# Performance work log

Hardware: AMD Instinct MI355X
Metric: run time of the kernel (lower is better)

The kernel has to match this reference:

```python
import jax, jax.numpy as jnp
import numpy as np

LR, HR, H, D1 = 512, 2048, 4, 200
N = 2 * HR            # 4096 nodes (fully connected graph)
C1 = D1 // H          # 50  per-head dim, layer 1
C2 = HR // H          # 512 per-head dim, layer 2
EPS = 1e-5


def setup_inputs() -> dict:
    key = jax.random.key(0)
    ks = jax.random.split(key, 24)
    lin = lambda k, fi, fo: jax.random.normal(k, (fi, fo), jnp.float32) * 0.02
    vec = lambda k, d: jax.random.normal(k, (d,), jnp.float32) * 0.02
    inp = {"lr_x": jax.random.normal(ks[0], (LR, N), jnp.float32)}
    # TransformerConv 1: lr -> 200 (query/key/value/skip linears, each with bias)
    inp["Wq1"], inp["bq1"] = lin(ks[1], LR, D1), vec(ks[2], D1)
    inp["Wk1"], inp["bk1"] = lin(ks[3], LR, D1), vec(ks[4], D1)
    inp["Wv1"], inp["bv1"] = lin(ks[5], LR, D1), vec(ks[6], D1)
    inp["Ws1"], inp["bs1"] = lin(ks[7], LR, D1), vec(ks[8], D1)
    # GraphNorm 1
    inp["gn1_w"] = 1.0 + 0.1 * jax.random.normal(ks[9], (D1,), jnp.float32)
    inp["gn1_b"] = vec(ks[10], D1)
    inp["gn1_ms"] = 1.0 + 0.1 * jax.random.normal(ks[11], (D1,), jnp.float32)
    # TransformerConv 2: 200 -> 2048
    inp["Wq2"], inp["bq2"] = lin(ks[12], D1, HR), vec(ks[13], HR)
    inp["Wk2"], inp["bk2"] = lin(ks[14], D1, HR), vec(ks[15], HR)
    inp["Wv2"], inp["bv2"] = lin(ks[16], D1, HR), vec(ks[17], HR)
    inp["Ws2"], inp["bs2"] = lin(ks[18], D1, HR), vec(ks[19], HR)
    # GraphNorm 2
    inp["gn2_w"] = 1.0 + 0.1 * jax.random.normal(ks[20], (HR,), jnp.float32)
    inp["gn2_b"] = vec(ks[21], HR)
    inp["gn2_ms"] = 1.0 + 0.1 * jax.random.normal(ks[22], (HR,), jnp.float32)
    return inp


def _transformer_conv(x, Wq, bq, Wk, bk, Wv, bv, Ws, bs, heads, ch):
    # PyG TransformerConv on a fully-connected edge_index == dense multi-head attention
    n = x.shape[0]
    q = (x @ Wq + bq).reshape(n, heads, ch)
    k = (x @ Wk + bk).reshape(n, heads, ch)
    v = (x @ Wv + bv).reshape(n, heads, ch)
    scores = jnp.einsum('ihc,jhc->hij', q, k) / (ch ** 0.5)  # [H, N, N]
    attn = jax.nn.softmax(scores, axis=-1)                   # softmax over source nodes j
    out = jnp.einsum('hij,jhc->ihc', attn, v).reshape(n, heads * ch)
    return out + x @ Ws + bs                                 # root/skip connection


def _graph_norm(x, w, b, ms):
    # PyG GraphNorm: y = w * (x - ms*mean) / sqrt(E[(x - ms*mean)^2] + eps) + b
    mean = jnp.mean(x, axis=0, keepdims=True)
    out = x - mean * ms
    var = jnp.mean(out * out, axis=0, keepdims=True)
    return out * jax.lax.rsqrt(var + EPS) * w + b


def reference(lr_x, Wq1, bq1, Wk1, bk1, Wv1, bv1, Ws1, bs1, gn1_w, gn1_b, gn1_ms,
              Wq2, bq2, Wk2, bk2, Wv2, bv2, Ws2, bs2, gn2_w, gn2_b, gn2_ms):
    h = _transformer_conv(lr_x.T, Wq1, bq1, Wk1, bk1, Wv1, bv1, Ws1, bs1, H, C1)  # [N, 200]
    h = _graph_norm(h, gn1_w, gn1_b, gn1_ms)
    h2 = _transformer_conv(h, Wq2, bq2, Wk2, bk2, Wv2, bv2, Ws2, bs2, H, C2)      # [N, HR]
    h2 = _graph_norm(h2, gn2_w, gn2_b, gn2_ms).T                                  # [HR, N]
    h2 = h2 / jnp.linalg.norm(h2, axis=1, keepdims=True)
    return jax.nn.relu(h2 @ h2.T)                                                 # [HR, HR]
```

## Files before the change

### kernel.cpp

```cpp
#include <hip/hip_runtime.h>
#include <math.h>

typedef unsigned int u32;
typedef unsigned short ushort_t;
typedef __attribute__((ext_vector_type(8))) short short8;
typedef __attribute__((ext_vector_type(4))) float f32x4;

#define PRIO(x) __builtin_amdgcn_s_setprio(x)

__device__ __forceinline__ ushort_t f2bf(float x) {
  u32 u = __float_as_uint(x);
  u32 r = (u + 0x7fffu + ((u >> 16) & 1u)) >> 16;
  return (ushort_t)r;
}
__device__ __forceinline__ float bf2f(u32 s) {
  return __uint_as_float(s << 16);
}
__device__ __forceinline__ void ld4bf(const ushort_t* p, float* o) {
  uint2 u = *(const uint2*)p;
  o[0] = bf2f(u.x & 0xffffu); o[1] = bf2f(u.x >> 16);
  o[2] = bf2f(u.y & 0xffffu); o[3] = bf2f(u.y >> 16);
}

__device__ __forceinline__ float block_sum256(float v, float* red) {
  #pragma unroll
  for (int o = 32; o > 0; o >>= 1) v += __shfl_down(v, o, 64);
  __syncthreads();
  if ((threadIdx.x & 63) == 0) red[threadIdx.x >> 6] = v;
  __syncthreads();
  return red[0] + red[1] + red[2] + red[3];
}

__global__ __launch_bounds__(256) void fused_attn1(
    const ushort_t* __restrict__ qk, const ushort_t* __restrict__ v,
    float* __restrict__ oP, float* __restrict__ r1p, float scale)
{
  __shared__ ushort_t Kl[2][4096];
  __shared__ ushort_t Vl[2][4096];
  __shared__ ushort_t Pl[128][80];
  const int t = threadIdx.x;
  const int lane = t & 63;
  const int wv = t >> 6;
  const int h = blockIdx.y;
  const int m0 = blockIdx.x * 128;
  const int z = blockIdx.z;
  const int lr = lane & 15;
  const int hk = lane >> 4;

  short8 aq[2][2];
  #pragma unroll
  for (int qb = 0; qb < 2; ++qb) {
    const ushort_t* qrow = qk + (size_t)(m0 + wv * 32 + qb * 16 + lr) * 512 + h * 64;
    aq[qb][0] = *(const short8*)(qrow + hk * 8);
    aq[qb][1] = *(const short8*)(qrow + 32 + hk * 8);
  }

  f32x4 oAcc[4][2];
  #pragma unroll
  for (int i = 0; i < 4; ++i) {
    oAcc[i][0] = (f32x4){0.f, 0.f, 0.f, 0.f};
    oAcc[i][1] = (f32x4){0.f, 0.f, 0.f, 0.f};
  }
  float racc[2][4] = {{0.f,0.f,0.f,0.f},{0.f,0.f,0.f,0.f}};

  const size_t kbase = (size_t)256 + h * 64;

  auto stage = [&](int buf, int n0) {
    #pragma unroll
    for (int i = 0; i < 2; ++i) {
      const int st = t + i * 256;
      const int row = st >> 3, cS = st & 7;
      const int lc = cS ^ (row & 7);
      __builtin_amdgcn_global_load_lds(
          (const __attribute__((address_space(1))) u32*)(qk + (size_t)(n0 + row) * 512 + kbase + lc * 8),
          (__attribute__((address_space(3))) u32*)(&Kl[buf][st * 8]), 16, 0, 0);
      __builtin_amdgcn_global_load_lds(
          (const __attribute__((address_space(1))) u32*)(v + (size_t)(h * 128 + row) * 4096 + n0 + lc * 8),
          (__attribute__((address_space(3))) u32*)(&Vl[buf][st * 8]), 16, 0, 0);
    }
  };

  stage(0, z * 1024);
  __syncthreads();

  int cur = 0;
  for (int it = 0; it < 16; ++it) {
    if (it + 1 < 16) stage(cur ^ 1, z * 1024 + (it + 1) * 64);
    #pragma unroll
    for (int nf = 0; nf < 4; ++nf) {
      const int rl = nf * 16 + lr;
      const char* kb = (const char*)&Kl[cur][0] + rl * 128;
      short8 b0 = *(const short8*)(kb + ((hk ^ (rl & 7)) * 16));
      short8 b1 = *(const short8*)(kb + (((4 + hk) ^ (rl & 7)) * 16));
      #pragma unroll
      for (int qb = 0; qb < 2; ++qb) {
        f32x4 sa = (f32x4){0.f, 0.f, 0.f, 0.f};
        PRIO(1);
        sa = __builtin_amdgcn_mfma_f32_16x16x32_bf16(aq[qb][0], b0, sa, 0, 0, 0);
        sa = __builtin_amdgcn_mfma_f32_16x16x32_bf16(aq[qb][1], b1, sa, 0, 0, 0);
        PRIO(0);
        #pragma unroll
        for (int r = 0; r < 4; ++r) {
          float e = exp2f(sa[r] * scale);
          racc[qb][r] += e;
          Pl[wv * 32 + qb * 16 + hk * 4 + r][nf * 16 + lr] = f2bf(e);
        }
      }
    }
    short8 ap[2][2];
    #pragma unroll
    for (int qb = 0; qb < 2; ++qb) {
      ap[qb][0] = *(const short8*)&Pl[wv * 32 + qb * 16 + lr][hk * 8];
      ap[qb][1] = *(const short8*)&Pl[wv * 32 + qb * 16 + lr][32 + hk * 8];
    }
    #pragma unroll
    for (int ff = 0; ff < 4; ++ff) {
      const int rl = ff * 16 + lr;
      const char* vb = (const char*)&Vl[cur][0] + rl * 128;
      short8 b0 = *(const short8*)(vb + ((hk ^ (rl & 7)) * 16));
      short8 b1 = *(const short8*)(vb + (((4 + hk) ^ (rl & 7)) * 16));
      PRIO(1);
      #pragma unroll
      for (int qb = 0; qb < 2; ++qb) {
        oAcc[ff][qb] = __builtin_amdgcn_mfma_f32_16x16x32_bf16(ap[qb][0], b0, oAcc[ff][qb], 0, 0, 0);
        oAcc[ff][qb] = __builtin_amdgcn_mfma_f32_16x16x32_bf16(ap[qb][1], b1, oAcc[ff][qb], 0, 0, 0);
      }
      PRIO(0);
    }
    __syncthreads();
    cur ^= 1;
  }

  #pragma unroll
  for (int qb = 0; qb < 2; ++qb) {
    #pragma unroll
    for (int r = 0; r < 4; ++r) {
      racc[qb][r] += __shfl_xor(racc[qb][r], 1);
      racc[qb][r] += __shfl_xor(racc[qb][r], 2);
      racc[qb][r] += __shfl_xor(racc[qb][r], 4);
      racc[qb][r] += __shfl_xor(racc[qb][r], 8);
    }
  }
  if (lr == 0) {
    float* rp = r1p + ((size_t)z * 4 + h) * 4096;
    #pragma unroll
    for (int qb = 0; qb < 2; ++qb)
      #pragma unroll
      for (int r = 0; r < 4; ++r)
        rp[m0 + wv * 32 + qb * 16 + hk * 4 + r] = racc[qb][r];
  }
  float* ob = oP + (size_t)z * 512 * 4096;
  #pragma unroll
  for (int ff = 0; ff < 4; ++ff) {
    const size_t fbase = (size_t)(h * 128 + ff * 16 + lr) * 4096;
    #pragma unroll
    for (int qb = 0; qb < 2; ++qb)
      #pragma unroll
      for (int r = 0; r < 4; ++r)
        ob[fbase + m0 + wv * 32 + qb * 16 + hk * 4 + r] = oAcc[ff][qb][r];
  }
}

__global__ __launch_bounds__(512, 2) void fused_attn2(
    const ushort_t* __restrict__ Tm, const ushort_t* __restrict__ X,
    const ushort_t* __restrict__ Xt, ushort_t* __restrict__ Up, float scale)
{
  __shared__ ushort_t Xl[16384];
  __shared__ ushort_t Xtl[2][16384];
  __shared__ ushort_t Pl[256][72];
  const int t = threadIdx.x;
  const int lane = t & 63;
  const int wv = t >> 6;
  const int h = blockIdx.y;
  const int m0 = blockIdx.x * 256;
  const int z = blockIdx.z;
  const int lr = lane & 15;
  const int hk = lane >> 4;

  short8 tq[2][7];
  #pragma unroll
  for (int qb = 0; qb < 2; ++qb) {
    const ushort_t* trow = Tm + ((size_t)h * 4096 + m0 + wv * 32 + qb * 16 + lr) * 256;
    #pragma unroll
    for (int s = 0; s < 7; ++s) tq[qb][s] = *(const short8*)(trow + s * 32 + hk * 8);
  }

  f32x4 uAcc[14][2];
  #pragma unroll
  for (int i = 0; i < 14; ++i) {
    uAcc[i][0] = (f32x4){0.f, 0.f, 0.f, 0.f};
    uAcc[i][1] = (f32x4){0.f, 0.f, 0.f, 0.f};
  }

  auto stageX = [&](int n0) {
    #pragma unroll
    for (int i = 0; i < 4; ++i) {
      const int st = t + i * 512;
      const int row = st >> 5, ph = st & 31;
      const int lc = (ph & 24) | ((ph & 7) ^ (row & 7));
      __builtin_amdgcn_global_load_lds(
          (const __attribute__((address_space(1))) u32*)(X + (size_t)(n0 + row) * 256 + lc * 8),
          (__attribute__((address_space(3))) u32*)(&Xl[st * 8]), 16, 0, 0);
    }
  };
  auto stageXt = [&](int buf, int n0) {
    #pragma unroll
    for (int i = 0; i < 4; ++i) {
      const int st = t + i * 512;
      const int row = st >> 3, ph = st & 7;
      const int lc = ph ^ (row & 7);
      __builtin_amdgcn_global_load_lds(
          (const __attribute__((address_space(1))) u32*)(Xt + (size_t)row * 4096 + n0 + lc * 8),
          (__attribute__((address_space(3))) u32*)(&Xtl[buf][st * 8]), 16, 0, 0);
    }
  };

  const int base = z * 16;
  stageX(base * 64);
  stageXt(0, base * 64);
  __syncthreads();

  int cur = 0;
  for (int it = 0; it < 16; ++it) {
    if (it + 1 < 16) stageXt(cur ^ 1, (base + it + 1) * 64);
    const char* xb = (const char*)&Xl[0];
    #pragma unroll
    for (int nf = 0; nf < 4; ++nf) {
      const int row = nf * 16 + lr;
      const char* rb = xb + row * 512;
      f32x4 sa0 = (f32x4){0.f, 0.f, 0.f, 0.f};
      f32x4 sa1 = (f32x4){0.f, 0.f, 0.f, 0.f};
      PRIO(1);
      #pragma unroll
      for (int s = 0; s < 7; ++s) {
        const int c = s * 4 + hk;
        const int ph = (c & 24) | ((c & 7) ^ (row & 7));
        short8 xf = *(const short8*)(rb + ph * 16);
        sa0 = __builtin_amdgcn_mfma_f32_16x16x32_bf16(xf, tq[0][s], sa0, 0, 0, 0);
        sa1 = __builtin_amdgcn_mfma_f32_16x16x32_bf16(xf, tq[1][s], sa1, 0, 0, 0);
      }
      PRIO(0);
      uint2 w0, w1;
      w0.x = (u32)f2bf(exp2f(sa0[0] * scale)) | ((u32)f2bf(exp2f(sa0[1] * scale)) << 16);
      w0.y = (u32)f2bf(exp2f(sa0[2] * scale)) | ((u32)f2bf(exp2f(sa0[3] * scale)) << 16);
      w1.x = (u32)f2bf(exp2f(sa1[0] * scale)) | ((u32)f2bf(exp2f(sa1[1] * scale)) << 16);
      w1.y = (u32)f2bf(exp2f(sa1[2] * scale)) | ((u32)f2bf(exp2f(sa1[3] * scale)) << 16);
      *(uint2*)((char*)&Pl[wv * 32 + lr][0] + nf * 32 + hk * 8) = w0;
      *(uint2*)((char*)&Pl[wv * 32 + 16 + lr][0] + nf * 32 + hk * 8) = w1;
    }
    __syncthreads();
    if (it + 1 < 16) stageX((base + it + 1) * 64);
    short8 p00 = *(const short8*)((const char*)&Pl[wv * 32 + lr][0] + hk * 16);
    short8 p01 = *(const short8*)((const char*)&Pl[wv * 32 + lr][0] + (4 + hk) * 16);
    short8 p10 = *(const short8*)((const char*)&Pl[wv * 32 + 16 + lr][0] + hk * 16);
    short8 p11 = *(const short8*)((const char*)&Pl[wv * 32 + 16 + lr][0] + (4 + hk) * 16);
    const char* xtb = (const char*)&Xtl[cur][0];
    #pragma unroll
    for (int ff = 0; ff < 14; ++ff) {
      const int row = ff * 16 + lr;
      const char* rb2 = xtb + row * 128;
      short8 x0 = *(const short8*)(rb2 + ((hk ^ (row & 7)) * 16));
      short8 x1 = *(const short8*)(rb2 + (((4 + hk) ^ (row & 7)) * 16));
      PRIO(1);
      uAcc[ff][0] = __builtin_amdgcn_mfma_f32_16x16x32_bf16(x0, p00, uAcc[ff][0], 0, 0, 0);
      uAcc[ff][0] = __builtin_amdgcn_mfma_f32_16x16x32_bf16(x1, p01, uAcc[ff][0], 0, 0, 0);
      uAcc[ff][1] = __builtin_amdgcn_mfma_f32_16x16x32_bf16(x0, p10, uAcc[ff][1], 0, 0, 0);
      uAcc[ff][1] = __builtin_amdgcn_mfma_f32_16x16x32_bf16(x1, p11, uAcc[ff][1], 0, 0, 0);
      PRIO(0);
    }
    __syncthreads();
    cur ^= 1;
  }

  ushort_t* ub = Up + (size_t)(z * 4 + h) * 256 * 4096;
  #pragma unroll
  for (int ff = 0; ff < 14; ++ff) {
    #pragma unroll
    for (int qb = 0; qb < 2; ++qb) {
      #pragma unroll
      for (int r = 0; r < 4; ++r) {
        const int a = ff * 16 + hk * 4 + r;
        ub[(size_t)a * 4096 + m0 + wv * 32 + qb * 16 + lr] = f2bf(uAcc[ff][qb][r]);
      }
    }
  }
}

__global__ __launch_bounds__(256) void combine_u(
    const ushort_t* __restrict__ Up, ushort_t* __restrict__ Usum,
    float* __restrict__ r2)
{
  __shared__ float tl[64][65];
  const int t = threadIdx.x;
  const int qt = blockIdx.x;
  const int at = blockIdx.y;
  const int h  = blockIdx.z;
  const int c = t & 63;
  const int rb = t >> 6;
  const size_t PLN = (size_t)4 * 256 * 4096;
  #pragma unroll
  for (int i = 0; i < 16; ++i) {
    const int r = rb + i * 4;
    const int a = at * 64 + r;
    const int q = qt * 64 + c;
    const size_t i0 = ((size_t)h * 256 + a) * 4096 + q;
    float val = bf2f(Up[i0]) + bf2f(Up[PLN + i0])
              + bf2f(Up[2 * PLN + i0]) + bf2f(Up[3 * PLN + i0]);
    tl[r][c] = val;
    if (a == 200) r2[(size_t)h * 4096 + q] = val;
  }
  __syncthreads();
  #pragma unroll
  for (int i = 0; i < 16; ++i) {
    const int r = rb + i * 4;
    const int q = qt * 64 + r;
    const int a = at * 64 + c;
    Usum[((size_t)h * 4096 + q) * 256 + a] = f2bf(tl[c][r]);
  }
}

#define RD_A(bb, mm, cc) (*(const short8*)(lsAc + (bb)*32768 + arow + (mm)*2048 + (cc)))
#define RD_B(bb, nn, cc) (*(const short8*)(lsBc + (bb)*32768 + brow + (nn)*2048 + (cc)))

#define MM8(nn, bv) { \
  acc[0][nn] = __builtin_amdgcn_mfma_f32_16x16x32_bf16(a0, bv, acc[0][nn], 0,0,0); \
  acc[1][nn] = __builtin_amdgcn_mfma_f32_16x16x32_bf16(a1, bv, acc[1][nn], 0,0,0); \
  acc[2][nn] = __builtin_amdgcn_mfma_f32_16x16x32_bf16(a2, bv, acc[2][nn], 0,0,0); \
  acc[3][nn] = __builtin_amdgcn_mfma_f32_16x16x32_bf16(a3, bv, acc[3][nn], 0,0,0); \
  acc[4][nn] = __builtin_amdgcn_mfma_f32_16x16x32_bf16(a4, bv, acc[4][nn], 0,0,0); \
  acc[5][nn] = __builtin_amdgcn_mfma_f32_16x16x32_bf16(a5, bv, acc[5][nn], 0,0,0); \
  acc[6][nn] = __builtin_amdgcn_mfma_f32_16x16x32_bf16(a6, bv, acc[6][nn], 0,0,0); \
  acc[7][nn] = __builtin_amdgcn_mfma_f32_16x16x32_bf16(a7, bv, acc[7][nn], 0,0,0); }

#define STG(BASE, LD, LS, bb, hf, tt) { \
  _Pragma("unroll") \
  for (int ii = 0; ii < 2; ++ii) { \
    const int s_ = t + ii * 512; \
    const int r_ = s_ >> 3; \
    const int lc_ = (s_ & 7) ^ (r_ & 7); \
    __builtin_amdgcn_global_load_lds( \
      (const __attribute__((address_space(1))) u32*)((BASE) + (size_t)((hf) * 128 + r_) * (LD) + (size_t)(tt) * 64 + lc_ * 8), \
      (__attribute__((address_space(3))) u32*)(&(LS)[bb][(hf) * 8192 + s_ * 8]), 16, 0, 0); \
  } }

#define BAR() __builtin_amdgcn_s_barrier()

#define GRP(bf, tS1, tS2) { \
  a0=RD_A(bf,0,c0); a1=RD_A(bf,1,c0); a2=RD_A(bf,2,c0); a3=RD_A(bf,3,c0); \
  a4=RD_A(bf,4,c0); a5=RD_A(bf,5,c0); a6=RD_A(bf,6,c0); a7=RD_A(bf,7,c0); \
  b0=RD_B(bf,0,c0); b1=RD_B(bf,1,c0); \
  STG(Ab, lda, lsA, 1-(bf), 1, tS1); STG(Bb, ldb, lsB, 1-(bf), 0, tS1); \
  BAR(); PRIO(1); MM8(0, b0); MM8(1, b1); PRIO(0); BAR(); \
  b2=RD_B(bf,2,c0); b3=RD_B(bf,3,c0); \
  STG(Bb, ldb, lsB, 1-(bf), 1, tS1); \
  BAR(); PRIO(1); MM8(2, b2); MM8(3, b3); PRIO(0); BAR(); \
  a0=RD_A(bf,0,c1); a1=RD_A(bf,1,c1); a2=RD_A(bf,2,c1); a3=RD_A(bf,3,c1); \
  a4=RD_A(bf,4,c1); a5=RD_A(bf,5,c1); a6=RD_A(bf,6,c1); a7=RD_A(bf,7,c1); \
  b0=RD_B(bf,0,c1); b1=RD_B(bf,1,c1); \
  BAR(); PRIO(1); MM8(0, b0); MM8(1, b1); PRIO(0); BAR(); \
  b2=RD_B(bf,2,c1); b3=RD_B(bf,3,c1); \
  STG(Ab, lda, lsA, (bf), 0, tS2); \
  BAR(); PRIO(1); MM8(2, b2); MM8(3, b3); PRIO(0); \
  asm volatile("s_waitcnt vmcnt(2)" ::: "memory"); \
  BAR(); }

template<int CMODE, bool RELU>
__global__ __launch_bounds__(512, 2) void mfma256_8ph(
    const ushort_t* __restrict__ A, const ushort_t* __restrict__ B,
    void* __restrict__ Cv, int lda, int ldb, int ldc,
    int K, int zsplit, size_t zA, size_t zB, size_t zC,
    int bShift, size_t bHead, int Mvalid, float scale)
{
  __shared__ ushort_t lsA[2][16384];
  __shared__ ushort_t lsB[2][16384];
  const int t = threadIdx.x;
  const int gx = gridDim.x;
  const int nwg = gx * gridDim.y;
  const int bid = blockIdx.y * gx + blockIdx.x;
  const int qq = nwg >> 3, rr_ = nwg & 7;
  const int xcd = bid & 7, idx = bid >> 3;
  const int swz = (xcd < rr_ ? xcd * (qq + 1) : rr_ * (qq + 1) + (xcd - rr_) * qq) + idx;
  const int m0 = (swz / gx) * 256;
  const int n0 = (swz % gx) * 256;
  const int z = blockIdx.z;
  int Kc = K, kOff = 0;
  size_t aZ = 0, bZ = 0, cZ = 0;
  if (zsplit > 1) { Kc = K / zsplit; kOff = z * Kc; cZ = (size_t)z * zC; }
  else { aZ = (size_t)z * zA; bZ = (size_t)z * zB; cZ = (size_t)z * zC; }
  const ushort_t* Ab = A + aZ + (size_t)m0 * lda + kOff;
  const ushort_t* Bb = B + bZ + (size_t)n0 * ldb + kOff
                     + (bShift >= 0 ? (size_t)(m0 >> bShift) * bHead : 0);
  const int NT = Kc / 64;

  f32x4 acc[8][4];
  #pragma unroll
  for (int i = 0; i < 8; ++i)
    #pragma unroll
    for (int j = 0; j < 4; ++j) acc[i][j] = (f32x4){0.f, 0.f, 0.f, 0.f};

  const int lane = t & 63;
  const int wv = t >> 6;
  const int wr = (wv >> 2) * 128;
  const int wc = (wv & 3) * 64;
  const int lr = lane & 15;
  const int kc = lane >> 4;
  const int sw = lane & 7;
  const int c0 = (kc ^ sw) * 16;
  const int c1 = c0 ^ 64;
  const int arow = (wr + lr) * 128;
  const int brow = (wc + lr) * 128;
  const char* lsAc = (const char*)lsA;
  const char* lsBc = (const char*)lsB;

  short8 a0, a1, a2, a3, a4, a5, a6, a7, b0, b1, b2, b3;

  STG(Ab, lda, lsA, 0, 0, 0); STG(Ab, lda, lsA, 0, 1, 0);
  STG(Bb, ldb, lsB, 0, 0, 0); STG(Bb, ldb, lsB, 0, 1, 0);
  STG(Ab, lda, lsA, 1, 0, 1);
  asm volatile("s_waitcnt vmcnt(2)" ::: "memory");
  BAR();

  const int NITER = NT >> 1;
  for (int it = 0; it < NITER; ++it) {
    const int tb = 2 * it;
    const int s1 = tb + 1;
    const int s2 = (tb + 2 < NT) ? tb + 2 : 0;
    const int s3 = (tb + 3 < NT) ? tb + 3 : 0;
    GRP(0, s1, s2)
    GRP(1, s2, s3)
  }

  const int row4 = (lane >> 4) * 4;
  const int coln = lane & 15;
  float* Cf = (float*)Cv + cZ;
  ushort_t* Ch = (ushort_t*)Cv + cZ;
  #pragma unroll
  for (int m = 0; m < 8; ++m) {
    #pragma unroll
    for (int r = 0; r < 4; ++r) {
      const int gm = m0 + wr + m * 16 + row4 + r;
      const bool ok = gm < Mvalid;
      #pragma unroll
      for (int n = 0; n < 4; ++n) {
        const int gn = n0 + wc + n * 16 + coln;
        float v = acc[m][n][r] * scale;
        if (RELU) v = fmaxf(v, 0.f);
        if (ok) {
          if (CMODE == 0)      Cf[(size_t)gm * ldc + gn] = v;
          else if (CMODE == 1) Ch[(size_t)gm * ldc + gn] = f2bf(v);
          else                 atomicAdd(&Cf[(size_t)gm * ldc + gn], v);
        }
      }
    }
  }
}

#undef GRP
#undef STG
#undef MM8
#undef RD_A
#undef RD_B

template<int CMODE, bool RELU>
__global__ __launch_bounds__(256) void mfma_bt(
    const ushort_t* __restrict__ A, const ushort_t* __restrict__ B,
    void* __restrict__ Cv, int lda, int ldb, int ldc,
    int K, int Ksplit, size_t zA, size_t zB, size_t zC,
    int bShift, size_t bHead, int mMask, int Mvalid, float scale)
{
  __shared__ ushort_t lsA[2][128 * 32];
  __shared__ ushort_t lsB[2][128 * 32];
  const int t  = threadIdx.x;
  const int m0 = blockIdx.y * 128;
  const int n0 = blockIdx.x * 128;
  const int z = blockIdx.z;
  int Kc = K, kOff = 0;
  size_t aZ = 0, bZ = 0, cZ = 0;
  if (Ksplit > 1) { Kc = K / Ksplit; kOff = z * Kc; cZ = (size_t)z * zC; }
  else { aZ = (size_t)z * zA; bZ = (size_t)z * zB; cZ = (size_t)z * zC; }
  const int NT = (Kc + 31) / 32;
  const ushort_t* Ab = A + aZ + (size_t)m0 * lda + kOff;
  const ushort_t* Bb = B + bZ + (size_t)n0 * ldb + kOff
                     + (bShift >= 0 ? (size_t)(m0 >> bShift) * bHead : 0);
  const int cs = t & 3;

  f32x4 acc[4][4];
  #pragma unroll
  for (int i = 0; i < 4; ++i)
    #pragma unroll
    for (int j = 0; j < 4; ++j) acc[i][j] = (f32x4){0.f, 0.f, 0.f, 0.f};

  const int lane = t & 63;
  const int wv = t >> 6;
  const int wr = (wv >> 1) * 64;
  const int wc = (wv & 1) * 64;
  const int lr = lane & 15;
  const int kc = lane >> 4;

  int roffA[4], roffB[4];
  #pragma unroll
  for (int m = 0; m < 4; ++m) {
    int ra = wr + m * 16 + lr;
    roffA[m] = ra * 64 + ((kc ^ (ra & 3)) * 16);
    int rb = wc + m * 16 + lr;
    roffB[m] = rb * 64 + ((kc ^ (rb & 3)) * 16);
  }

  auto stage = [&](int buf, int kt) {
    const ushort_t* As = Ab + kt * 32;
    const ushort_t* Bs = Bb + kt * 32;
    #pragma unroll
    for (int i = 0; i < 2; ++i) {
      int s = t + i * 256;
      int r = s >> 2;
      int c = cs ^ (r & 3);
      __builtin_amdgcn_global_load_lds(
          (const __attribute__((address_space(1))) u32*)(As + (size_t)r * lda + c * 8),
          (__attribute__((address_space(3))) u32*)(&lsA[buf][s * 8]), 16, 0, 0);
    }
    #pragma unroll
    for (int i = 0; i < 2; ++i) {
      int s = t + i * 256;
      int r = s >> 2;
      int c = cs ^ (r & 3);
      __builtin_amdgcn_global_load_lds(
          (const __attribute__((address_space(1))) u32*)(Bs + (size_t)r * ldb + c * 8),
          (__attribute__((address_space(3))) u32*)(&lsB[buf][s * 8]), 16, 0, 0);
    }
  };

  stage(0, 0);
  __syncthreads();
  int cur = 0;
  for (int kt = 0; kt < NT; ++kt) {
    if (kt + 1 < NT) stage(cur ^ 1, kt + 1);
    short8 af[4], bfr[4];
    const char* baseA = (const char*)&lsA[cur][0];
    const char* baseB = (const char*)&lsB[cur][0];
    #pragma unroll
    for (int m = 0; m < 4; ++m) af[m]  = *(const short8*)(baseA + roffA[m]);
    #pragma unroll
    for (int n = 0; n < 4; ++n) bfr[n] = *(const short8*)(baseB + roffB[n]);
    PRIO(1);
    #pragma unroll
    for (int m = 0; m < 4; ++m)
      #pragma unroll
      for (int n = 0; n < 4; ++n)
        acc[m][n] = __builtin_amdgcn_mfma_f32_16x16x32_bf16(af[m], bfr[n], acc[m][n], 0, 0, 0);
    PRIO(0);
    __syncthreads();
    cur ^= 1;
  }

  const int row4 = (lane >> 4) * 4;
  const int coln = lane & 15;
  float* Cf = (float*)Cv + cZ;
  ushort_t* Ch = (ushort_t*)Cv + cZ;
  #pragma unroll
  for (int m = 0; m < 4; ++m) {
    #pragma unroll
    for (int r = 0; r < 4; ++r) {
      const int gm = m0 + wr + m * 16 + row4 + r;
      const bool ok = (mMask >= 0) ? ((gm & mMask) < Mvalid) : (gm < Mvalid);
      #pragma unroll
      for (int n = 0; n < 4; ++n) {
        const int gn = n0 + wc + n * 16 + coln;
        float v = acc[m][n][r] * scale;
        if (RELU) v = fmaxf(v, 0.f);
        if (ok) {
          if (CMODE == 0)      Cf[(size_t)gm * ldc + gn] = v;
          else if (CMODE == 1) Ch[(size_t)gm * ldc + gn] = f2bf(v);
          else                 atomicAdd(&Cf[(size_t)gm * ldc + gn], v);
        }
      }
    }
  }
}

__global__ __launch_bounds__(256) void wt_conv(
    const float* __restrict__ W, const float* __restrict__ bias,
    ushort_t* __restrict__ dst, int Mtot, int ldw, int Kv, int Kp,
    int PADH, int VALH)
{
  const int m = blockIdx.x;
  const int h = m / PADH, c0 = m % PADH;
  const int fout = h * VALH + c0;
  const bool valid = (c0 < VALH) && (fout < Mtot);
  for (int k = threadIdx.x; k < Kp; k += blockDim.x) {
    float v = 0.f;
    if (valid) {
      if (k < Kv) v = W[(size_t)k * ldw + fout];
      else if (k == Kv) v = bias[fout];
    }
    dst[(size_t)m * Kp + k] = f2bf(v);
  }
}

__global__ __launch_bounds__(256) void wt_trans(
    const float* __restrict__ W, const float* __restrict__ bias,
    ushort_t* __restrict__ dst)
{
  const int rid = blockIdx.x;
  const int h = rid >> 8, a = rid & 255;
  for (int f = threadIdx.x; f < 512; f += 256) {
    float v = 0.f;
    if (a < 200)       v = W[(size_t)a * 2048 + h * 512 + f];
    else if (a == 200) v = bias[h * 512 + f];
    dst[(size_t)rid * 512 + f] = f2bf(v);
  }
}

__global__ __launch_bounds__(256) void xt_conv(
    const float* __restrict__ h1nT, ushort_t* __restrict__ Xt)
{
  const int a = blockIdx.x;
  for (int q = threadIdx.x; q < 4096; q += 256) {
    float v = (a < 200) ? h1nT[(size_t)a * 4096 + q] : ((a == 200) ? 1.f : 0.f);
    Xt[(size_t)a * 4096 + q] = f2bf(v);
  }
}

__global__ __launch_bounds__(256) void trans_pad(
    const float* __restrict__ src, ushort_t* __restrict__ dst, int Kv, int Kp)
{
  __shared__ float tl[64][65];
  const int t = threadIdx.x;
  const int f0 = blockIdx.x * 64;
  const int i0 = blockIdx.y * 64;
  const int c = t & 63, rbase = t >> 6;
  #pragma unroll
  for (int it = 0; it < 16; ++it) {
    int r = rbase + it * 4;
    int f = f0 + r;
    tl[r][c] = (f < Kv) ? src[(size_t)f * 4096 + i0 + c] : 0.f;
  }
  __syncthreads();
  #pragma unroll
  for (int it = 0; it < 16; ++it) {
    int r = rbase + it * 4;
    int f = f0 + c;
    if (f < Kp) {
      float v = (f < Kv) ? tl[c][r] : ((f == Kv) ? 1.f : 0.f);
      dst[(size_t)(i0 + r) * Kp + f] = f2bf(v);
    }
  }
}

__global__ __launch_bounds__(256) void graph_norm_attn1(
    const ushort_t* __restrict__ skip, const float* __restrict__ oP,
    const float* __restrict__ r1p, float* __restrict__ out,
    const float* __restrict__ w, const float* __restrict__ b,
    const float* __restrict__ ms)
{
  __shared__ float red[4];
  const int t = threadIdx.x;
  const int row = blockIdx.x;
  const int h = row / 50;
  const int pr = h * 128 + row % 50;
  const ushort_t* sk = skip + (size_t)pr * 4096;
  const size_t OSTR = (size_t)512 * 4096;
  float v[16];
  float s = 0.f;
  #pragma unroll
  for (int e = 0; e < 4; ++e) {
    const int idx = t * 4 + 1024 * e;
    float a[4];
    ld4bf(&sk[idx], a);
    float4 o0 = *(const float4*)&oP[(size_t)pr * 4096 + idx];
    float4 o1 = *(const float4*)&oP[OSTR + (size_t)pr * 4096 + idx];
    float4 o2 = *(const float4*)&oP[2 * OSTR + (size_t)pr * 4096 + idx];
    float4 o3 = *(const float4*)&oP[3 * OSTR + (size_t)pr * 4096 + idx];
    float4 r0 = *(const float4*)&r1p[(size_t)h * 4096 + idx];
    float4 r1 = *(const float4*)&r1p[(size_t)(4 + h) * 4096 + idx];
    float4 r2 = *(const float4*)&r1p[(size_t)(8 + h) * 4096 + idx];
    float4 r3 = *(const float4*)&r1p[(size_t)(12 + h) * 4096 + idx];
    v[e*4+0] = a[0] + (o0.x + o1.x + o2.x + o3.x) / (r0.x + r1.x + r2.x + r3.x);
    v[e*4+1] = a[1] + (o0.y + o1.y + o2.y + o3.y) / (r0.y + r1.y + r2.y + r3.y);
    v[e*4+2] = a[2] + (o0.z + o1.z + o2.z + o3.z) / (r0.z + r1.z + r2.z + r3.z);
    v[e*4+3] = a[3] + (o0.w + o1.w + o2.w + o3.w) / (r0.w + r1.w + r2.w + r3.w);
    s += v[e*4+0] + v[e*4+1] + v[e*4+2] + v[e*4+3];
  }
  const float mean = block_sum256(s, red) * (1.f / 4096.f);
  const float sub = mean * ms[row];
  float s2 = 0.f;
  #pragma unroll
  for (int e = 0; e < 16; ++e) { v[e] -= sub; s2 += v[e] * v[e]; }
  const float var = block_sum256(s2, red) * (1.f / 4096.f);
  const float scl = rsqrtf(var + 1e-5f) * w[row];
  const float bb = b[row];
  float* y = out + (size_t)row * 4096;
  #pragma unroll
  for (int e = 0; e < 4; ++e) {
    float o0[4];
    #pragma unroll
    for (int q = 0; q < 4; ++q) o0[q] = v[e * 4 + q] * scl + bb;
    *(float4*)&y[t * 4 + 1024 * e] = *(float4*)&o0[0];
  }
}

__global__ __launch_bounds__(256) void graph_norm_attn2(
    const ushort_t* __restrict__ skip, const ushort_t* __restrict__ O,
    const float* __restrict__ r2, ushort_t* __restrict__ out,
    const float* __restrict__ w, const float* __restrict__ b,
    const float* __restrict__ ms)
{
  __shared__ float red[4];
  const int t = threadIdx.x;
  const int row = blockIdx.x;
  const ushort_t* sk = skip + (size_t)row * 4096;
  const ushort_t* pa = O + (size_t)row * 4096;
  const float* rr = r2 + (size_t)(row >> 9) * 4096;
  float v[16];
  float s = 0.f;
  #pragma unroll
  for (int e = 0; e < 4; ++e) {
    const int idx = t * 4 + 1024 * e;
    float a[4], oa[4];
    ld4bf(&sk[idx], a); ld4bf(&pa[idx], oa);
    float4 rv = *(const float4*)&rr[idx];
    v[e*4+0] = a[0] + oa[0] / rv.x;
    v[e*4+1] = a[1] + oa[1] / rv.y;
    v[e*4+2] = a[2] + oa[2] / rv.z;
    v[e*4+3] = a[3] + oa[3] / rv.w;
    s += v[e*4+0] + v[e*4+1] + v[e*4+2] + v[e*4+3];
  }
  const float mean = block_sum256(s, red) * (1.f / 4096.f);
  const float sub = mean * ms[row];
  float s2 = 0.f;
  #pragma unroll
  for (int e = 0; e < 16; ++e) { v[e] -= sub; s2 += v[e] * v[e]; }
  const float var = block_sum256(s2, red) * (1.f / 4096.f);
  const float scl = rsqrtf(var + 1e-5f) * w[row];
  const float bb = b[row];
  #pragma unroll
  for (int e = 0; e < 16; ++e) v[e] = v[e] * scl + bb;
  float s3 = 0.f;
  #pragma unroll
  for (int e = 0; e < 16; ++e) s3 += v[e] * v[e];
  const float osc = rsqrtf(block_sum256(s3, red));
  ushort_t* y = out + (size_t)row * 4096;
  #pragma unroll
  for (int e = 0; e < 4; ++e) {
    ushort_t o0[4];
    #pragma unroll
    for (int q = 0; q < 4; ++q) o0[q] = f2bf(v[e * 4 + q] * osc);
    *(ushort2*)&y[t * 4 + 1024 * e] = *(ushort2*)&o0[0];
    *(ushort2*)&y[t * 4 + 1024 * e + 2] = *(ushort2*)&o0[2];
  }
}

__global__ __launch_bounds__(256) void add4_relu_bf16(
    const ushort_t* __restrict__ g, float* __restrict__ out)
{
  const size_t i = (size_t)blockIdx.x * 256 + threadIdx.x;
  const size_t ss = (size_t)2048 * 2048;
  float a[4], b[4], c[4], d[4];
  ld4bf(&g[i * 4], a);
  ld4bf(&g[ss + i * 4], b);
  ld4bf(&g[2 * ss + i * 4], c);
  ld4bf(&g[3 * ss + i * 4], d);
  float4 o;
  o.x = fmaxf(a[0] + b[0] + c[0] + d[0], 0.f);
  o.y = fmaxf(a[1] + b[1] + c[1] + d[1], 0.f);
  o.z = fmaxf(a[2] + b[2] + c[2] + d[2], 0.f);
  o.w = fmaxf(a[3] + b[3] + c[3] + d[3], 0.f);
  ((float4*)out)[i] = o;
}

extern "C" void kernel_launch(void* const* d_in, const int* in_sizes, int n_in,
                              void* d_out, int out_size, void* d_ws, size_t ws_size,
                              hipStream_t stream)
{
  (void)in_sizes; (void)n_in; (void)out_size; (void)ws_size;
  const float* lr_x = (const float*)d_in[0];
  const float* Wq1 = (const float*)d_in[1];  const float* bq1 = (const float*)d_in[2];
  const float* Wk1 = (const float*)d_in[3];  const float* bk1 = (const float*)d_in[4];
  const float* Wv1 = (const float*)d_in[5];  const float* bv1 = (const float*)d_in[6];
  const float* Ws1 = (const float*)d_in[7];  const float* bs1 = (const float*)d_in[8];
  const float* gn1w = (const float*)d_in[9]; const float* gn1b = (const float*)d_in[10];
  const float* gn1ms = (const float*)d_in[11];
  const float* Wq2 = (const float*)d_in[12]; const float* bq2 = (const float*)d_in[13];
  const float* Wk2 = (const float*)d_in[14]; const float* bk2 = (const float*)d_in[15];
  const float* Wv2 = (const float*)d_in[16]; const float* bv2 = (const float*)d_in[17];
  const float* Ws2 = (const float*)d_in[18]; const float* bs2 = (const float*)d_in[19];
  const float* gn2w = (const float*)d_in[20]; const float* gn2b = (const float*)d_in[21];
  const float* gn2ms = (const float*)d_in[22];

  char* p = (char*)d_ws;
  auto alloc = [&](size_t bytes) { char* r = p; p += (bytes + 255) & ~(size_t)255; return r; };
  char*     scrA = alloc((size_t)32 * 1024 * 1024);
  ushort_t* xb   = (ushort_t*)alloc((size_t)4096 * 544 * 2);
  ushort_t* qk1b = (ushort_t*)alloc((size_t)4096 * 512 * 2);
  ushort_t* v1s  = (ushort_t*)alloc((size_t)1024 * 4096 * 2);
  char*     u0   = alloc((size_t)16 * 1024 * 1024);
  float*    h1nT = (float*)   alloc((size_t)200 * 4096 * 4);
  ushort_t* h1nb = (ushort_t*)alloc((size_t)4096 * 256 * 2);
  ushort_t* Wqk1 = (ushort_t*)alloc((size_t)512 * 544 * 2);
  ushort_t* Wvs1 = (ushort_t*)alloc((size_t)1024 * 544 * 2);
  ushort_t* Wcat = (ushort_t*)alloc((size_t)4096 * 256 * 2);
  ushort_t* Qt   = (ushort_t*)alloc((size_t)4 * 256 * 512 * 2);
  ushort_t* Kt   = (ushort_t*)alloc((size_t)4 * 256 * 512 * 2);
  ushort_t* Mtall= (ushort_t*)alloc((size_t)4 * 256 * 256 * 2);
  ushort_t* Tall = (ushort_t*)alloc((size_t)4 * 4096 * 256 * 2);
  ushort_t* Xtb  = (ushort_t*)alloc((size_t)256 * 4096 * 2);
  ushort_t* vs2b = (ushort_t*)alloc((size_t)4096 * 4096 * 2);
  ushort_t* Usum = (ushort_t*)alloc((size_t)4 * 4096 * 256 * 2);
  ushort_t* Opl  = (ushort_t*)alloc((size_t)2048 * 4096 * 2);
  float*    r1p  = (float*)   alloc((size_t)16 * 4096 * 4);
  float*    r2   = (float*)   alloc((size_t)4 * 4096 * 4);
  float*    oP   = (float*)scrA;
  ushort_t* UpH  = (ushort_t*)scrA;
  ushort_t* g4   = (ushort_t*)scrA;
  ushort_t* h2b  = (ushort_t*)u0;

  const dim3 b256(256, 1, 1);
  const dim3 b512(512, 1, 1);
  const float LOG2E = 1.4426950408889634f;
  const float sc1e = 0.14142135623730951f * LOG2E;
  const float sc2e = 0.04419417382415922f * LOG2E;

  wt_conv<<<dim3(256),  b256, 0, stream>>>(Wq1, bq1, Wqk1,             200, 200, 512, 544, 64, 50);
  wt_conv<<<dim3(256),  b256, 0, stream>>>(Wk1, bk1, Wqk1 + 256 * 544, 200, 200, 512, 544, 64, 50);
  wt_conv<<<dim3(512),  b256, 0, stream>>>(Wv1, bv1, Wvs1,             200, 200, 512, 544, 128, 50);
  wt_conv<<<dim3(512),  b256, 0, stream>>>(Ws1, bs1, Wvs1 + 512 * 544, 200, 200, 512, 544, 128, 50);
  wt_conv<<<dim3(2048), b256, 0, stream>>>(Wv2, bv2, Wcat,              2048, 2048, 200, 256, 2048, 2048);
  wt_conv<<<dim3(2048), b256, 0, stream>>>(Ws2, bs2, Wcat + 2048 * 256, 2048, 2048, 200, 256, 2048, 2048);
  wt_trans<<<dim3(1024), b256, 0, stream>>>(Wq2, bq2, Qt);
  wt_trans<<<dim3(1024), b256, 0, stream>>>(Wk2, bk2, Kt);
  trans_pad<<<dim3(9, 64), b256, 0, stream>>>(lr_x, xb, 512, 544);

  mfma_bt<1, false><<<dim3(4, 32), b256, 0, stream>>>(
      xb, Wqk1, qk1b, 544, 544, 512, 544, 1, 0, 0, 0, -1, 0, -1, 4096, 1.f);
  mfma_bt<1, false><<<dim3(32, 8), b256, 0, stream>>>(
      Wvs1, xb, v1s, 544, 544, 4096, 544, 1, 0, 0, 0, -1, 0, -1, 1024, 1.f);

  fused_attn1<<<dim3(32, 4, 4), b256, 0, stream>>>(qk1b, v1s, oP, r1p, sc1e);
  graph_norm_attn1<<<dim3(200), b256, 0, stream>>>(
      v1s + (size_t)512 * 4096, oP, r1p, h1nT, gn1w, gn1b, gn1ms);
  trans_pad<<<dim3(4, 64), b256, 0, stream>>>(h1nT, h1nb, 200, 256);
  xt_conv<<<dim3(256), b256, 0, stream>>>(h1nT, Xtb);

  mfma_bt<1, false><<<dim3(32, 32), b256, 0, stream>>>(
      Wcat, h1nb, vs2b, 256, 256, 4096, 224, 1, 0, 0, 0, -1, 0, -1, 4096, 1.f);

  mfma_bt<1, false><<<dim3(2, 2, 4), b256, 0, stream>>>(
      Kt, Qt, Mtall, 512, 512, 256, 512, 1,
      (size_t)256 * 512, (size_t)256 * 512, (size_t)256 * 256, -1, 0, -1, 256, 1.f);
  mfma_bt<1, false><<<dim3(2, 32, 4), b256, 0, stream>>>(
      h1nb, Mtall, Tall, 256, 256, 256, 224, 1,
      0, (size_t)256 * 256, (size_t)4096 * 256, -1, 0, -1, 4096, 1.f);
  fused_attn2<<<dim3(16, 4, 4), b512, 0, stream>>>(Tall, h1nb, Xtb, UpH, sc2e);
  combine_u<<<dim3(64, 4, 4), b256, 0, stream>>>(UpH, Usum, r2);
  mfma_bt<1, false><<<dim3(32, 16), b256, 0, stream>>>(
      Wcat, Usum, Opl, 256, 256, 4096, 224, 1,
      0, 0, 0, 9, (size_t)4096 * 256, -1, 2048, 1.f);
  graph_norm_attn2<<<dim3(2048), b256, 0, stream>>>(
      vs2b + (size_t)2048 * 4096, Opl, r2, h2b, gn2w, gn2b, gn2ms);

  mfma256_8ph<1, false><<<dim3(8, 8, 4), b512, 0, stream>>>(
      h2b, h2b, g4, 4096, 4096, 2048, 4096, 4,
      0, 0, (size_t)2048 * 2048, -1, 0, 2048, 1.f);
  add4_relu_bf16<<<dim3(4096), b256, 0, stream>>>(g4, (float*)d_out);
}
```

Measured before the change: 325.4 us.

## Store attention partials in bf16, merge weight conversion launches, fuse Xt padding into norm

```diff
diff --git a/kernel.cpp b/kernel.cpp
--- a/kernel.cpp
+++ b/kernel.cpp
@@ -33,7 +33,7 @@
 
 __global__ __launch_bounds__(256) void fused_attn1(
     const ushort_t* __restrict__ qk, const ushort_t* __restrict__ v,
-    float* __restrict__ oP, float* __restrict__ r1p, float scale)
+    ushort_t* __restrict__ oP, float* __restrict__ r1p, float scale)
 {
   __shared__ ushort_t Kl[2][4096];
   __shared__ ushort_t Vl[2][4096];
@@ -149,15 +149,18 @@
       for (int r = 0; r < 4; ++r)
         rp[m0 + wv * 32 + qb * 16 + hk * 4 + r] = racc[qb][r];
   }
-  float* ob = oP + (size_t)z * 512 * 4096;
+  ushort_t* ob = oP + (size_t)z * 512 * 4096;
   #pragma unroll
   for (int ff = 0; ff < 4; ++ff) {
     const size_t fbase = (size_t)(h * 128 + ff * 16 + lr) * 4096;
     #pragma unroll
-    for (int qb = 0; qb < 2; ++qb)
-      #pragma unroll
-      for (int r = 0; r < 4; ++r)
-        ob[fbase + m0 + wv * 32 + qb * 16 + hk * 4 + r] = oAcc[ff][qb][r];
+    for (int qb = 0; qb < 2; ++qb) {
+      const int q0 = m0 + wv * 32 + qb * 16 + hk * 4;
+      uint2 w;
+      w.x = (u32)f2bf(oAcc[ff][qb][0]) | ((u32)f2bf(oAcc[ff][qb][1]) << 16);
+      w.y = (u32)f2bf(oAcc[ff][qb][2]) | ((u32)f2bf(oAcc[ff][qb][3]) << 16);
+      *(uint2*)&ob[fbase + q0] = w;
+    }
   }
 }
 
@@ -577,11 +580,14 @@
   }
 }
 
-__global__ __launch_bounds__(256) void wt_conv(
-    const float* __restrict__ W, const float* __restrict__ bias,
-    ushort_t* __restrict__ dst, int Mtot, int ldw, int Kv, int Kp,
-    int PADH, int VALH)
-{
+__global__ __launch_bounds__(256) void wt_conv2(
+    const float* __restrict__ W0, const float* __restrict__ b0v, ushort_t* __restrict__ d0,
+    const float* __restrict__ W1, const float* __restrict__ b1v, ushort_t* __restrict__ d1,
+    int Mtot, int ldw, int Kv, int Kp, int PADH, int VALH)
+{
+  const float* W = blockIdx.y ? W1 : W0;
+  const float* bias = blockIdx.y ? b1v : b0v;
+  ushort_t* dst = blockIdx.y ? d1 : d0;
   const int m = blockIdx.x;
   const int h = m / PADH, c0 = m % PADH;
   const int fout = h * VALH + c0;
@@ -596,10 +602,13 @@
   }
 }
 
-__global__ __launch_bounds__(256) void wt_trans(
-    const float* __restrict__ W, const float* __restrict__ bias,
-    ushort_t* __restrict__ dst)
-{
+__global__ __launch_bounds__(256) void wt_trans2(
+    const float* __restrict__ W0, const float* __restrict__ b0v, ushort_t* __restrict__ d0,
+    const float* __restrict__ W1, const float* __restrict__ b1v, ushort_t* __restrict__ d1)
+{
+  const float* W = blockIdx.y ? W1 : W0;
+  const float* bias = blockIdx.y ? b1v : b0v;
+  ushort_t* dst = blockIdx.y ? d1 : d0;
   const int rid = blockIdx.x;
   const int h = rid >> 8, a = rid & 255;
   for (int f = threadIdx.x; f < 512; f += 256) {
@@ -610,16 +619,6 @@
   }
 }
 
-__global__ __launch_bounds__(256) void xt_conv(
-    const float* __restrict__ h1nT, ushort_t* __restrict__ Xt)
-{
-  const int a = blockIdx.x;
-  for (int q = threadIdx.x; q < 4096; q += 256) {
-    float v = (a < 200) ? h1nT[(size_t)a * 4096 + q] : ((a == 200) ? 1.f : 0.f);
-    Xt[(size_t)a * 4096 + q] = f2bf(v);
-  }
-}
-
 __global__ __launch_bounds__(256) void trans_pad(
     const float* __restrict__ src, ushort_t* __restrict__ dst, int Kv, int Kp)
 {
@@ -646,15 +645,41 @@
   }
 }
 
+__global__ __launch_bounds__(256) void transb(
+    const ushort_t* __restrict__ Xt, ushort_t* __restrict__ dst)
+{
+  __shared__ ushort_t tl[64][68];
+  const int t = threadIdx.x;
+  const int a0 = blockIdx.x * 64;
+  const int q0 = blockIdx.y * 64;
+  const int c = t & 63, rb = t >> 6;
+  #pragma unroll
+  for (int i = 0; i < 16; ++i) {
+    const int r = rb + i * 4;
+    tl[r][c] = Xt[(size_t)(a0 + r) * 4096 + q0 + c];
+  }
+  __syncthreads();
+  #pragma unroll
+  for (int i = 0; i < 16; ++i) {
+    const int r = rb + i * 4;
+    dst[(size_t)(q0 + r) * 256 + a0 + c] = tl[c][r];
+  }
+}
+
 __global__ __launch_bounds__(256) void graph_norm_attn1(
-    const ushort_t* __restrict__ skip, const float* __restrict__ oP,
-    const float* __restrict__ r1p, float* __restrict__ out,
+    const ushort_t* __restrict__ skip, const ushort_t* __restrict__ oP,
+    const float* __restrict__ r1p, ushort_t* __restrict__ outXt,
     const float* __restrict__ w, const float* __restrict__ b,
     const float* __restrict__ ms)
 {
-  __shared__ float red[4];
   const int t = threadIdx.x;
   const int row = blockIdx.x;
+  if (row >= 200) {
+    const ushort_t val = (row == 200) ? f2bf(1.f) : (ushort_t)0;
+    for (int q = t; q < 4096; q += 256) outXt[(size_t)row * 4096 + q] = val;
+    return;
+  }
+  __shared__ float red[4];
   const int h = row / 50;
   const int pr = h * 128 + row % 50;
   const ushort_t* sk = skip + (size_t)pr * 4096;
@@ -664,20 +689,20 @@
   #pragma unroll
   for (int e = 0; e < 4; ++e) {
     const int idx = t * 4 + 1024 * e;
-    float a[4];
+    float a[4], o0[4], o1[4], o2[4], o3[4];
     ld4bf(&sk[idx], a);
-    float4 o0 = *(const float4*)&oP[(size_t)pr * 4096 + idx];
-    float4 o1 = *(const float4*)&oP[OSTR + (size_t)pr * 4096 + idx];
-    float4 o2 = *(const float4*)&oP[2 * OSTR + (size_t)pr * 4096 + idx];
-    float4 o3 = *(const float4*)&oP[3 * OSTR + (size_t)pr * 4096 + idx];
+    ld4bf(&oP[(size_t)pr * 4096 + idx], o0);
+    ld4bf(&oP[OSTR + (size_t)pr * 4096 + idx], o1);
+    ld4bf(&oP[2 * OSTR + (size_t)pr * 4096 + idx], o2);
+    ld4bf(&oP[3 * OSTR + (size_t)pr * 4096 + idx], o3);
     float4 r0 = *(const float4*)&r1p[(size_t)h * 4096 + idx];
     float4 r1 = *(const float4*)&r1p[(size_t)(4 + h) * 4096 + idx];
     float4 r2 = *(const float4*)&r1p[(size_t)(8 + h) * 4096 + idx];
     float4 r3 = *(const float4*)&r1p[(size_t)(12 + h) * 4096 + idx];
-    v[e*4+0] = a[0] + (o0.x + o1.x + o2.x + o3.x) / (r0.x + r1.x + r2.x + r3.x);
-    v[e*4+1] = a[1] + (o0.y + o1.y + o2.y + o3.y) / (r0.y + r1.y + r2.y + r3.y);
-    v[e*4+2] = a[2] + (o0.z + o1.z + o2.z + o3.z) / (r0.z + r1.z + r2.z + r3.z);
-    v[e*4+3] = a[3] + (o0.w + o1.w + o2.w + o3.w) / (r0.w + r1.w + r2.w + r3.w);
+    v[e*4+0] = a[0] + (o0[0] + o1[0] + o2[0] + o3[0]) / (r0.x + r1.x + r2.x + r3.x);
+    v[e*4+1] = a[1] + (o0[1] + o1[1] + o2[1] + o3[1]) / (r0.y + r1.y + r2.y + r3.y);
+    v[e*4+2] = a[2] + (o0[2] + o1[2] + o2[2] + o3[2]) / (r0.z + r1.z + r2.z + r3.z);
+    v[e*4+3] = a[3] + (o0[3] + o1[3] + o2[3] + o3[3]) / (r0.w + r1.w + r2.w + r3.w);
     s += v[e*4+0] + v[e*4+1] + v[e*4+2] + v[e*4+3];
   }
   const float mean = block_sum256(s, red) * (1.f / 4096.f);
@@ -688,13 +713,14 @@
   const float var = block_sum256(s2, red) * (1.f / 4096.f);
   const float scl = rsqrtf(var + 1e-5f) * w[row];
   const float bb = b[row];
-  float* y = out + (size_t)row * 4096;
+  ushort_t* y = outXt + (size_t)row * 4096;
   #pragma unroll
   for (int e = 0; e < 4; ++e) {
-    float o0[4];
-    #pragma unroll
-    for (int q = 0; q < 4; ++q) o0[q] = v[e * 4 + q] * scl + bb;
-    *(float4*)&y[t * 4 + 1024 * e] = *(float4*)&o0[0];
+    const int idx = t * 4 + 1024 * e;
+    uint2 wd;
+    wd.x = (u32)f2bf(v[e*4+0] * scl + bb) | ((u32)f2bf(v[e*4+1] * scl + bb) << 16);
+    wd.y = (u32)f2bf(v[e*4+2] * scl + bb) | ((u32)f2bf(v[e*4+3] * scl + bb) << 16);
+    *(uint2*)&y[idx] = wd;
   }
 }
 
@@ -793,7 +819,6 @@
   ushort_t* qk1b = (ushort_t*)alloc((size_t)4096 * 512 * 2);
   ushort_t* v1s  = (ushort_t*)alloc((size_t)1024 * 4096 * 2);
   char*     u0   = alloc((size_t)16 * 1024 * 1024);
-  float*    h1nT = (float*)   alloc((size_t)200 * 4096 * 4);
   ushort_t* h1nb = (ushort_t*)alloc((size_t)4096 * 256 * 2);
   ushort_t* Wqk1 = (ushort_t*)alloc((size_t)512 * 544 * 2);
   ushort_t* Wvs1 = (ushort_t*)alloc((size_t)1024 * 544 * 2);
@@ -808,7 +833,7 @@
   ushort_t* Opl  = (ushort_t*)alloc((size_t)2048 * 4096 * 2);
   float*    r1p  = (float*)   alloc((size_t)16 * 4096 * 4);
   float*    r2   = (float*)   alloc((size_t)4 * 4096 * 4);
-  float*    oP   = (float*)scrA;
+  ushort_t* oP   = (ushort_t*)scrA;
   ushort_t* UpH  = (ushort_t*)scrA;
   ushort_t* g4   = (ushort_t*)scrA;
   ushort_t* h2b  = (ushort_t*)u0;
@@ -819,14 +844,13 @@
   const float sc1e = 0.14142135623730951f * LOG2E;
   const float sc2e = 0.04419417382415922f * LOG2E;
 
-  wt_conv<<<dim3(256),  b256, 0, stream>>>(Wq1, bq1, Wqk1,             200, 200, 512, 544, 64, 50);
-  wt_conv<<<dim3(256),  b256, 0, stream>>>(Wk1, bk1, Wqk1 + 256 * 544, 200, 200, 512, 544, 64, 50);
-  wt_conv<<<dim3(512),  b256, 0, stream>>>(Wv1, bv1, Wvs1,             200, 200, 512, 544, 128, 50);
-  wt_conv<<<dim3(512),  b256, 0, stream>>>(Ws1, bs1, Wvs1 + 512 * 544, 200, 200, 512, 544, 128, 50);
-  wt_conv<<<dim3(2048), b256, 0, stream>>>(Wv2, bv2, Wcat,              2048, 2048, 200, 256, 2048, 2048);
-  wt_conv<<<dim3(2048), b256, 0, stream>>>(Ws2, bs2, Wcat + 2048 * 256, 2048, 2048, 200, 256, 2048, 2048);
-  wt_trans<<<dim3(1024), b256, 0, stream>>>(Wq2, bq2, Qt);
-  wt_trans<<<dim3(1024), b256, 0, stream>>>(Wk2, bk2, Kt);
+  wt_conv2<<<dim3(256, 2), b256, 0, stream>>>(
+      Wq1, bq1, Wqk1, Wk1, bk1, Wqk1 + 256 * 544, 200, 200, 512, 544, 64, 50);
+  wt_conv2<<<dim3(512, 2), b256, 0, stream>>>(
+      Wv1, bv1, Wvs1, Ws1, bs1, Wvs1 + 512 * 544, 200, 200, 512, 544, 128, 50);
+  wt_conv2<<<dim3(2048, 2), b256, 0, stream>>>(
+      Wv2, bv2, Wcat, Ws2, bs2, Wcat + 2048 * 256, 2048, 2048, 200, 256, 2048, 2048);
+  wt_trans2<<<dim3(1024, 2), b256, 0, stream>>>(Wq2, bq2, Qt, Wk2, bk2, Kt);
   trans_pad<<<dim3(9, 64), b256, 0, stream>>>(lr_x, xb, 512, 544);
 
   mfma_bt<1, false><<<dim3(4, 32), b256, 0, stream>>>(
@@ -835,10 +859,9 @@
       Wvs1, xb, v1s, 544, 544, 4096, 544, 1, 0, 0, 0, -1, 0, -1, 1024, 1.f);
 
   fused_attn1<<<dim3(32, 4, 4), b256, 0, stream>>>(qk1b, v1s, oP, r1p, sc1e);
-  graph_norm_attn1<<<dim3(200), b256, 0, stream>>>(
-      v1s + (size_t)512 * 4096, oP, r1p, h1nT, gn1w, gn1b, gn1ms);
-  trans_pad<<<dim3(4, 64), b256, 0, stream>>>(h1nT, h1nb, 200, 256);
-  xt_conv<<<dim3(256), b256, 0, stream>>>(h1nT, Xtb);
+  graph_norm_attn1<<<dim3(256), b256, 0, stream>>>(
+      v1s + (size_t)512 * 4096, oP, r1p, Xtb, gn1w, gn1b, gn1ms);
+  transb<<<dim3(4, 64), b256, 0, stream>>>(Xtb, h1nb);
 
   mfma_bt<1, false><<<dim3(32, 32), b256, 0, stream>>>(
       Wcat, h1nb, vs2b, 256, 256, 4096, 224, 1, 0, 0, 0, -1, 0, -1, 4096, 1.f);
```

New measurement: 304.3 us. -6.5%, faster.
